# Performance work log

Hardware: AMD Instinct MI355X
Metric: run time of the kernel (lower is better)

The kernel has to match this reference:

```python
import jax, jax.numpy as jnp
import numpy as np
from jax import lax

K = 100
NUM_CLASSES = 80
MIN_X = 1; MIN_Y = 1; MAX_X = 4; MAX_Y = 4   # int(base_layer_range/16) for [16,64,16,64]
KEEP = 300
IOU_TH = 0.5
ROI_H = 2 * MAX_Y + 1  # 9
ROI_W = 2 * MAX_X + 1  # 9
MASK_OUT = 36          # 9 -> two stride-2 deconvs -> 36
SCALE = (36.0 - 1.0) / (9.0 - 1.0)
BN_INV = 1.0 / np.sqrt(1.0 + 1e-3)  # BN eval, running mean 0 / var 1, eps=1e-3
SIZES = [(64, 64), (32, 32), (16, 16)]


def bilinear(img, xx, yy):
    # img [..., H, W]; xx, yy same shape S; border-clamped bilinear sample -> [..., *S]
    H, W = img.shape[-2], img.shape[-1]
    xx = jnp.clip(xx, 0.0, W - 1.0)
    yy = jnp.clip(yy, 0.0, H - 1.0)
    x0f = jnp.floor(xx); y0f = jnp.floor(yy)
    wx = xx - x0f; wy = yy - y0f
    x0 = x0f.astype(jnp.int32); y0 = y0f.astype(jnp.int32)
    x1 = jnp.minimum(x0 + 1, W - 1); y1 = jnp.minimum(y0 + 1, H - 1)
    v00 = img[..., y0, x0]; v01 = img[..., y0, x1]
    v10 = img[..., y1, x0]; v11 = img[..., y1, x1]
    return (1 - wy) * ((1 - wx) * v00 + wx * v01) + wy * ((1 - wx) * v10 + wx * v11)


def roi_align(feat, boxes):
    # feat [C,H,W], boxes [N,4] in feat coords -> [N,C,ROI_H,ROI_W] (sampling_ratio=1)
    n = boxes.shape[0]
    x1, y1, x2, y2 = boxes[:, 0], boxes[:, 1], boxes[:, 2], boxes[:, 3]
    jx = (jnp.arange(ROI_W, dtype=jnp.float32) + 0.5) / ROI_W
    jy = (jnp.arange(ROI_H, dtype=jnp.float32) + 0.5) / ROI_H
    gx = x1[:, None] + (x2 - x1)[:, None] * jx  # [N,ROI_W]
    gy = y1[:, None] + (y2 - y1)[:, None] * jy  # [N,ROI_H]
    xx = jnp.broadcast_to(gx[:, None, :], (n, ROI_H, ROI_W))
    yy = jnp.broadcast_to(gy[:, :, None], (n, ROI_H, ROI_W))
    out = bilinear(feat, xx, yy)  # [C,N,ROI_H,ROI_W]
    return jnp.transpose(out, (1, 0, 2, 3))


def crop_resize(masks, boxes):
    # masks [N,h,w], boxes [N,4] -> [N,MASK_OUT,MASK_OUT]
    n = boxes.shape[0]
    t = jnp.arange(MASK_OUT, dtype=jnp.float32) / (MASK_OUT - 1.0)
    x1, y1, x2, y2 = boxes[:, 0], boxes[:, 1], boxes[:, 2], boxes[:, 3]
    gx = x1[:, None] + (x2 - x1)[:, None] * t
    gy = y1[:, None] + (y2 - y1)[:, None] * t
    xx = jnp.broadcast_to(gx[:, None, :], (n, MASK_OUT, MASK_OUT))
    yy = jnp.broadcast_to(gy[:, :, None], (n, MASK_OUT, MASK_OUT))
    return jax.vmap(bilinear)(masks, xx, yy)


def nms_keep(boxes, scores):
    # greedy NMS, faithful to torchvision semantics; returns bool keep flags [N]
    n = boxes.shape[0]
    x1, y1, x2, y2 = boxes[:, 0], boxes[:, 1], boxes[:, 2], boxes[:, 3]
    area = (x2 - x1) * (y2 - y1)
    ix1 = jnp.maximum(x1[:, None], x1[None, :]); iy1 = jnp.maximum(y1[:, None], y1[None, :])
    ix2 = jnp.minimum(x2[:, None], x2[None, :]); iy2 = jnp.minimum(y2[:, None], y2[None, :])
    inter = jnp.clip(ix2 - ix1, 0.0) * jnp.clip(iy2 - iy1, 0.0)
    iou = inter / (area[:, None] + area[None, :] - inter + 1e-9)
    order = jnp.argsort(-scores)  # stable
    def step(carry, idx):
        supp, keep = carry
        k = jnp.logical_not(supp[idx])
        keep = keep.at[idx].set(k)
        supp = jnp.logical_or(supp, jnp.logical_and(k, iou[idx] > IOU_TH))
        return (supp, keep), None
    init = (jnp.zeros((n,), bool), jnp.zeros((n,), bool))
    (_, keep), _ = lax.scan(step, init, order)
    return keep


def _conv(x, w, b, pad):
    y = lax.conv_general_dilated(x, w, (1, 1), [(pad, pad), (pad, pad)],
                                 dimension_numbers=('NCHW', 'OIHW', 'NCHW'))
    return y + b[None, :, None, None]


def _deconv(x, w, b):
    # ConvTranspose2d(k=2, s=2): fractionally-strided conv, doubles spatial size
    y = lax.conv_general_dilated(x, w, (1, 1), [(1, 1), (1, 1)], lhs_dilation=(2, 2),
                                 dimension_numbers=('NCHW', 'OIHW', 'NCHW'))
    return y + b[None, :, None, None]


def _bn(x, g, b):
    return x * (g * BN_INV)[None, :, None, None] + b[None, :, None, None]


def mask_head(x, c1_w, c1_b, mid_w, mid_b, bn_g, bn_b, d1_w, d1_b, d2_w, d2_b, c5_w, c5_b, c6_w, c6_b):
    r = jax.nn.relu
    h = r(_bn(_conv(x, c1_w, c1_b, 1), bn_g[0], bn_b[0]))
    for j in range(3):  # conv2..conv4
        h = r(_bn(_conv(h, mid_w[j], mid_b[j], 1), bn_g[1 + j], bn_b[1 + j]))
    h = r(_deconv(h, d1_w, d1_b))
    h = r(_bn(_conv(h, c5_w, c5_b, 1), bn_g[4], bn_b[4]))
    h = r(_deconv(h, d2_w, d2_b))
    return jax.nn.sigmoid(_conv(h, c6_w, c6_b, 0))


def _decode_layer(heat, tlr, brr, i, H0, W0):
    C, H, W = heat.shape
    hw = H * W
    scores, inds = lax.top_k(heat.reshape(-1), K)
    clses = (inds // hw).astype(jnp.float32)
    rem = inds % hw
    ys = (rem // W).astype(jnp.float32)
    xs = (rem % W).astype(jnp.float32)
    t = tlr.reshape(2, hw)[:, rem]  # [2,K]
    b = brr.reshape(2, hw)[:, rem]
    rx = float(MAX_X - MIN_X); ry = float(MAX_Y - MIN_Y)
    cx = (MAX_X + MIN_X) / 2.0;  cy = (MAX_Y + MIN_Y) / 2.0
    tlx = jnp.clip(xs - (rx * t[0] + cx), 0.0, float(W))
    tly = jnp.clip(ys - (ry * t[1] + cy), 0.0, float(H))
    brx = jnp.clip(xs + (rx * b[0] + cx), 0.0, float(W))
    bry = jnp.clip(ys + (ry * b[1] + cy), 0.0, float(H))
    boxes = jnp.stack([tlx, tly, brx, bry], 1)
    sc = jnp.where((brx < tlx) | (bry < tly), -1.0, scores)
    mb = jnp.stack([xs - MAX_X, ys - MAX_Y, xs + MAX_X, ys + MAX_Y,
                    jnp.full((K,), float(i))], 1)
    s2, order = lax.top_k(sc, K)  # num_dets(1000) >= K -> full sort by score
    boxes = boxes[order]; mb = mb[order]; cls = clses[order]
    lay = jnp.full((K,), float(i))
    cols = jnp.stack([s2, s2, lay, cls], 1)
    bws = jnp.concatenate([boxes, cols], 1)  # boxes_without_scaling [K,8]
    scale = jnp.array([W0 / W, H0 / H, W0 / W, H0 / H], jnp.float32)
    dets = jnp.concatenate([boxes * scale, cols], 1)
    return dets, bws, mb


def _decode_one(h0, h1, h2, t0, t1, t2, b0, b1, b2, f0, f1, f2,
                c1_w, c1_b, mid_w, mid_b, bn_g, bn_b, d1_w, d1_b, d2_w, d2_b,
                c5_w, c5_b, c6_w, c6_b):
    heats = (h0, h1, h2); tls = (t0, t1, t2); brs = (b0, b1, b2); feats = (f0, f1, f2)
    H0, W0 = heats[0].shape[1], heats[0].shape[2]
    dets_l, bws_l, mb_l = [], [], []
    for i in range(3):
        d, bw, mb = _decode_layer(heats[i], tls[i], brs[i], i, H0, W0)
        dets_l.append(d); bws_l.append(bw); mb_l.append(mb)
    dets = jnp.concatenate(dets_l, 0)   # [300,8]
    bws = jnp.concatenate(bws_l, 0)
    mb = jnp.concatenate(mb_l, 0)       # [300,5]
    # NMS faithful to source: boxes = detections[:,1:5], scores = detections[:,4]
    keep = nms_keep(dets[:, 1:5], dets[:, 4])
    sel = jnp.argsort(-jnp.where(keep, dets[:, 4], -1e9))[:KEEP]
    dets = dets[sel]; bws = bws[sel]; mb = mb[sel]
    # sort by mask layer index descending (features processed last->first)
    ord2 = jnp.argsort(-mb[:, 4])
    dets = dets[ord2]; bws = bws[ord2]; mb = mb[ord2]
    # ROI pool each box from its own layer's feature map
    pooled = jnp.stack([roi_align(feats[i], mb[:, :4]) for i in range(3)], 0)  # [3,N,C,9,9]
    lay = jnp.clip(mb[:, 4].astype(jnp.int32), 0, 2)
    rois = pooled[lay, jnp.arange(KEEP)]  # [N,256,9,9]
    masks_all = mask_head(rois, c1_w, c1_b, mid_w, mid_b, bn_g, bn_b,
                          d1_w, d1_b, d2_w, d2_b, c5_w, c5_b, c6_w, c6_b)  # [N,80,36,36]
    cls = jnp.clip(dets[:, 7].astype(jnp.int32), 0, NUM_CLASSES - 1)
    masks = masks_all[jnp.arange(KEEP), cls]  # [N,36,36] (one-hot scatter/select)
    bws4 = bws[:, :4] - jnp.tile(mb[:, :2], (1, 2))
    norm_boxes = SCALE * bws4
    masks = crop_resize(masks, norm_boxes)
    return dets, masks


def setup_inputs():
    key = jax.random.key(0)
    ks = jax.random.split(key, 32)
    B = 1
    inp = {}
    for i, (H, W) in enumerate(SIZES):
        inp['heat%d' % i] = jax.random.uniform(ks[i], (B, NUM_CLASSES, H, W), jnp.float32)
        inp['tl%d' % i] = 0.1 * jax.random.normal(ks[3 + i], (B, 2, H, W), jnp.float32)
        inp['br%d' % i] = 0.1 * jax.random.normal(ks[6 + i], (B, 2, H, W), jnp.float32)
        inp['feat%d' % i] = jax.random.normal(ks[9 + i], (B, 256, H, W), jnp.float32)
    inp['c1_w'] = 0.05 * jax.random.normal(ks[12], (256, 256, 3, 3), jnp.float32)
    inp['c1_b'] = jnp.zeros((256,), jnp.float32)
    inp['mid_w'] = 0.05 * jax.random.normal(ks[13], (3, 256, 256, 3, 3), jnp.float32)
    inp['mid_b'] = jnp.zeros((3, 256), jnp.float32)
    inp['bn_g'] = jnp.ones((5, 256), jnp.float32)
    inp['bn_b'] = jnp.zeros((5, 256), jnp.float32)
    inp['d1_w'] = 0.05 * jax.random.normal(ks[14], (256, 256, 2, 2), jnp.float32)
    inp['d1_b'] = jnp.zeros((256,), jnp.float32)
    inp['d2_w'] = 0.05 * jax.random.normal(ks[15], (256, 256, 2, 2), jnp.float32)
    inp['d2_b'] = jnp.zeros((256,), jnp.float32)
    inp['c5_w'] = 0.05 * jax.random.normal(ks[16], (256, 256, 3, 3), jnp.float32)
    inp['c5_b'] = jnp.zeros((256,), jnp.float32)
    inp['c6_w'] = 0.05 * jax.random.normal(ks[17], (NUM_CLASSES, 256, 1, 1), jnp.float32)
    inp['c6_b'] = jnp.zeros((NUM_CLASSES,), jnp.float32)
    return inp


def reference(heat0, heat1, heat2, tl0, tl1, tl2, br0, br1, br2, feat0, feat1, feat2,
              c1_w, c1_b, mid_w, mid_b, bn_g, bn_b, d1_w, d1_b, d2_w, d2_b,
              c5_w, c5_b, c6_w, c6_b):
    dets, masks = jax.vmap(_decode_one, in_axes=(0,) * 12 + (None,) * 14)(
        heat0, heat1, heat2, tl0, tl1, tl2, br0, br1, br2, feat0, feat1, feat2,
        c1_w, c1_b, mid_w, mid_b, bn_g, bn_b, d1_w, d1_b, d2_w, d2_b, c5_w, c5_b, c6_w, c6_b)
    return dets, masks  # [B,300,8], [B,300,36,36]
```

## Files before the change

### kernel.cpp

```cpp
#include <hip/hip_runtime.h>
#include <math.h>

typedef __attribute__((ext_vector_type(8))) short bf16x8;
typedef __attribute__((ext_vector_type(4))) float f32x4;

__device__ __forceinline__ unsigned fkey_u(float v){
  unsigned b = __float_as_uint(v);
  return (b & 0x80000000u) ? ~b : (b | 0x80000000u);
}
__device__ __forceinline__ float fkey_inv(unsigned m){
  unsigned b = (m & 0x80000000u) ? (m & 0x7fffffffu) : ~m;
  return __uint_as_float(b);
}
__device__ __forceinline__ unsigned short f2bf(float f){
  unsigned u = __float_as_uint(f);
  unsigned r = (u + 0x7fffu + ((u>>16)&1u)) >> 16;
  return (unsigned short)r;
}
__device__ __forceinline__ unsigned long long shfl_xor_u64(unsigned long long v, int mask){
  int lo = __shfl_xor((int)(unsigned)(v & 0xFFFFFFFFull), mask, 64);
  int hi = __shfl_xor((int)(unsigned)(v >> 32), mask, 64);
  return ((unsigned long long)(unsigned)hi << 32) | (unsigned long long)(unsigned)lo;
}
__device__ __forceinline__ unsigned long long bshfl_u64(unsigned long long v, int lane){
  int lo = __shfl((int)(unsigned)(v & 0xFFFFFFFFull), lane, 64);
  int hi = __shfl((int)(unsigned)(v >> 32), lane, 64);
  return ((unsigned long long)(unsigned)hi << 32) | (unsigned long long)(unsigned)lo;
}
#define BNI 0.9995003746877732f

template<int E, int J>
__device__ __forceinline__ void reg_step(unsigned long long* key, int t, int k2){
  #pragma unroll
  for (int r=0;r<E;r++){
    if ((r & J)==0){
      int e = t*E + r;
      bool desc = ((e & k2)==0);
      unsigned long long a=key[r], b=key[r^J];
      if (desc ? (a<b) : (a>b)){ key[r]=b; key[r^J]=a; }
    }
  }
}
template<int E>
__device__ __forceinline__ void reg_tail(unsigned long long* key, int t, int k2, int jstart){
  if constexpr (E>=8) { if (jstart>=4) reg_step<E,4>(key,t,k2); }
  if constexpr (E>=4) { if (jstart>=2) reg_step<E,2>(key,t,k2); }
  if (jstart>=1) reg_step<E,1>(key,t,k2);
}
template<int E>
__device__ void bitonic_desc(unsigned long long* key, unsigned long long* lds){
  const int t = threadIdx.x;
  const int N = E*256;
  for (int k2=2;k2<=N;k2<<=1){
    for (int j=k2>>1; j>=E; j>>=1){
      int w = j/E;
      bool lower = ((t & w)==0);
      bool desc  = (((t*E) & k2)==0);
      bool keep_max = (desc == lower);
      if (w < 64){
        #pragma unroll
        for (int r=0;r<E;r++){
          unsigned long long mine=key[r];
          unsigned long long o=shfl_xor_u64(mine, w);
          bool gt = mine > o;
          key[r] = keep_max ? (gt?mine:o) : (gt?o:mine);
        }
      } else {
        __syncthreads();
        #pragma unroll
        for (int r=0;r<E;r++) lds[t*E+r]=key[r];
        __syncthreads();
        #pragma unroll
        for (int r=0;r<E;r++){
          unsigned long long mine=key[r];
          unsigned long long o=lds[(t*E+r)^j];
          bool gt = mine > o;
          key[r] = keep_max ? (gt?mine:o) : (gt?o:mine);
        }
      }
    }
    int jstart = ((k2>>1) < (E>>1)) ? (k2>>1) : (E>>1);
    reg_tail<E>(key,t,k2,jstart);
  }
  __syncthreads();
  #pragma unroll
  for (int r=0;r<E;r++) lds[t*E+r]=key[r];
  __syncthreads();
}

__global__ __launch_bounds__(256) void k_sel1(
    const float* __restrict__ h0, const float* __restrict__ h1, const float* __restrict__ h2,
    unsigned long long* __restrict__ c1)
{
  int b = blockIdx.x;
  int layer, chunk;
  if (b < 320){ layer=0; chunk=b; }
  else if (b < 400){ layer=1; chunk=b-320; }
  else { layer=2; chunk=b-400; }
  const float* heat = (layer==0)?h0:((layer==1)?h1:h2);
  __shared__ unsigned long long lds[1024];
  unsigned long long key[4];
  int t = threadIdx.x;
  int base = chunk*1024 + t*4;
  float4 v = *(const float4*)(heat + base);
  key[0] = ((unsigned long long)fkey_u(v.x)<<32) | (unsigned long long)(0xFFFFFFFFu - (unsigned)(base+0));
  key[1] = ((unsigned long long)fkey_u(v.y)<<32) | (unsigned long long)(0xFFFFFFFFu - (unsigned)(base+1));
  key[2] = ((unsigned long long)fkey_u(v.z)<<32) | (unsigned long long)(0xFFFFFFFFu - (unsigned)(base+2));
  key[3] = ((unsigned long long)fkey_u(v.w)<<32) | (unsigned long long)(0xFFFFFFFFu - (unsigned)(base+3));
  bitonic_desc<4>(key, lds);
  if (t<100) c1[(size_t)b*100 + t] = lds[t];
}

__global__ __launch_bounds__(256) void k_sel2(
    const unsigned long long* __restrict__ c1, unsigned long long* __restrict__ c2)
{
  int b = blockIdx.x;
  __shared__ unsigned long long lds[2048];
  unsigned long long key[8];
  int t=threadIdx.x;
  const unsigned long long* src = c1 + (size_t)b*2000;
  #pragma unroll
  for (int r=0;r<8;r++){
    int i=t*8+r;
    key[r] = (i<2000)? src[i] : 0ull;
  }
  bitonic_desc<8>(key, lds);
  if (t<100) c2[(size_t)b*100+t]=lds[t];
}

__global__ __launch_bounds__(256) void k_sel3_decode(
    const unsigned long long* __restrict__ c2,
    const float* __restrict__ tl0,const float* __restrict__ tl1,const float* __restrict__ tl2,
    const float* __restrict__ br0,const float* __restrict__ br1,const float* __restrict__ br2,
    float* __restrict__ dets, float* __restrict__ bws, float* __restrict__ mbw)
{
  int layer = blockIdx.x;
  int hw = 4096 >> (layer*2);
  int W = 64>>layer;
  float Wf = (float)W;
  const float* tl = (layer==0)?tl0:((layer==1)?tl1:tl2);
  const float* br = (layer==0)?br0:((layer==1)?br1:br2);
  int base = (layer==0)?0:((layer==1)?1600:2000);
  int cnt  = (layer==0)?1600:((layer==1)?400:100);
  __shared__ unsigned long long lds[2048];
  __shared__ float scl[100];
  unsigned long long key[8];
  int t = threadIdx.x;
  #pragma unroll
  for (int r=0;r<8;r++){
    int i=t*8+r;
    key[r] = (i<cnt)? c2[base+i] : 0ull;
  }
  bitonic_desc<8>(key, lds);
  unsigned long long kwin=0;
  if (t<100) kwin = lds[t];
  float tlx=0,tly=0,brx=0,bry=0,xs=0,ys=0,clsfv=0,scv=0;
  if (t<100){
    unsigned m=(unsigned)(kwin>>32);
    unsigned gidx = 0xFFFFFFFFu - (unsigned)(kwin & 0xFFFFFFFFull);
    float val = fkey_inv(m);
    int cls = (int)(gidx / (unsigned)hw);
    int rem = (int)(gidx % (unsigned)hw);
    int iy = rem / W, ix = rem % W;
    xs = (float)ix; ys = (float)iy; clsfv = (float)cls;
    float t0=tl[rem], t1=tl[hw+rem], b0=br[rem], b1=br[hw+rem];
    tlx = fminf(fmaxf(xs - (3.0f*t0 + 2.5f), 0.0f), Wf);
    tly = fminf(fmaxf(ys - (3.0f*t1 + 2.5f), 0.0f), Wf);
    brx = fminf(fmaxf(xs + (3.0f*b0 + 2.5f), 0.0f), Wf);
    bry = fminf(fmaxf(ys + (3.0f*b1 + 2.5f), 0.0f), Wf);
    scv = ((brx<tlx)||(bry<tly)) ? -1.0f : val;
    scl[t]=scv;
  }
  __syncthreads();
  if (t<100){
    int rank=0;
    for (int i=0;i<100;i++){
      float si=scl[i];
      rank += ((si>scv)||(si==scv && i<t)) ? 1 : 0;
    }
    int row = layer*100 + rank;
    float sx = (float)(1<<layer);
    float* dr = dets + row*8;
    dr[0]=tlx*sx; dr[1]=tly*sx; dr[2]=brx*sx; dr[3]=bry*sx;
    dr[4]=scv; dr[5]=scv; dr[6]=(float)layer; dr[7]=clsfv;
    float* bwr = bws + row*8;
    bwr[0]=tlx;bwr[1]=tly;bwr[2]=brx;bwr[3]=bry;bwr[4]=scv;bwr[5]=scv;bwr[6]=(float)layer;bwr[7]=clsfv;
    float* mr = mbw + row*5;
    mr[0]=xs-4.0f; mr[1]=ys-4.0f; mr[2]=xs+4.0f; mr[3]=ys+4.0f; mr[4]=(float)layer;
  }
}

#define NMS_STEP(P, OC, M) { \
  int idx=__shfl((OC),(P),64); \
  unsigned long long supw=bshfl_u64(sup, idx>>6); \
  int kq=(int)((~(supw>>(idx&63)))&1ull); \
  if (t==0) keep_[idx]=kq; \
  unsigned long long v0=bshfl_u64(M[0],(P)); \
  unsigned long long v1=bshfl_u64(M[1],(P)); \
  unsigned long long v2=bshfl_u64(M[2],(P)); \
  unsigned long long v3=bshfl_u64(M[3],(P)); \
  unsigned long long v4=bshfl_u64(M[4],(P)); \
  unsigned long long mv=(t==0)?v0:((t==1)?v1:((t==2)?v2:((t==3)?v3:((t==4)?v4:0ull)))); \
  if (kq) sup|=mv; }

__global__ __launch_bounds__(320) void k_nms(
    const float* __restrict__ dets, const float* __restrict__ bws, const float* __restrict__ mbw,
    float* __restrict__ out_dets, float* __restrict__ mbf, int* __restrict__ clsf,
    int* __restrict__ layf, float* __restrict__ nbox)
{
  __shared__ __align__(16) float4 bq[300];
  __shared__ __align__(16) float sc[300];
  __shared__ __align__(16) float kk[300];
  __shared__ __align__(16) float lq[300];
  __shared__ float lyv[300];
  __shared__ unsigned long long sm_ord[300][5];
  __shared__ int order_[300], keep_[300], sel_[300], fperm[300];
  int t = threadIdx.x;
  float X1=0,Y1=0,X2=0,Y2=0,S=0,A=0;
  if (t<300){
    const float* r = dets + t*8;
    X1=r[1];Y1=r[2];X2=r[3];Y2=r[4];
    S=r[4];
    A=(X2-X1)*(Y2-Y1);
    bq[t]=make_float4(X1,Y1,X2,Y2);
    sc[t]=S;
    lyv[t]=mbw[t*5+4];
  }
  __syncthreads();
  if (t<300){
    int rank=0;
    for (int j4=0;j4<75;j4++){
      float4 s4=*(const float4*)&sc[j4*4];
      int j=j4*4;
      rank += ((s4.x>S)||(s4.x==S&&(j+0)<t)) ? 1:0;
      rank += ((s4.y>S)||(s4.y==S&&(j+1)<t)) ? 1:0;
      rank += ((s4.z>S)||(s4.z==S&&(j+2)<t)) ? 1:0;
      rank += ((s4.w>S)||(s4.w==S&&(j+3)<t)) ? 1:0;
    }
    unsigned long long wrow[5];
    #pragma unroll
    for (int jw=0;jw<5;jw++){
      unsigned long long bits=0;
      int lim=(jw==4)?44:64;
      for (int jj=0;jj<lim;jj++){
        int j=jw*64+jj;
        float4 q=bq[j];
        float aj=(q.z-q.x)*(q.w-q.y);
        float ix1=fmaxf(X1,q.x), iy1=fmaxf(Y1,q.y);
        float ix2=fminf(X2,q.z), iy2=fminf(Y2,q.w);
        float it=fmaxf(ix2-ix1,0.f)*fmaxf(iy2-iy1,0.f);
        float iou=it/(A+aj-it+1e-9f);
        bits |= ((unsigned long long)(iou>0.5f))<<jj;
      }
      wrow[jw]=bits;
    }
    order_[rank]=t;
    #pragma unroll
    for (int q=0;q<5;q++) sm_ord[rank][q]=wrow[q];
  }
  __syncthreads();
  if (t<64){
    int o0=order_[t], o1=order_[64+t], o2=order_[128+t], o3=order_[192+t];
    int o4=(t<44)? order_[256+t] : 0;
    unsigned long long m0[5],m1[5],m2[5],m3[5],m4[5];
    #pragma unroll
    for (int q=0;q<5;q++){
      m0[q]=sm_ord[t][q]; m1[q]=sm_ord[64+t][q];
      m2[q]=sm_ord[128+t][q]; m3[q]=sm_ord[192+t][q];
      m4[q]=(t<44)? sm_ord[256+t][q] : 0ull;
    }
    unsigned long long sup=0;
    for (int p=0;p<64;p++) NMS_STEP(p,o0,m0);
    for (int p=0;p<64;p++) NMS_STEP(p,o1,m1);
    for (int p=0;p<64;p++) NMS_STEP(p,o2,m2);
    for (int p=0;p<64;p++) NMS_STEP(p,o3,m3);
    for (int p=0;p<44;p++) NMS_STEP(p,o4,m4);
  }
  __syncthreads();
  if (t<300) kk[t] = keep_[t] ? sc[t] : -1000000000.0f;
  __syncthreads();
  float KV=0; int rank2=0;
  if (t<300){
    KV=kk[t];
    for (int j4=0;j4<75;j4++){
      float4 s4=*(const float4*)&kk[j4*4];
      int j=j4*4;
      rank2 += ((s4.x>KV)||(s4.x==KV&&(j+0)<t)) ? 1:0;
      rank2 += ((s4.y>KV)||(s4.y==KV&&(j+1)<t)) ? 1:0;
      rank2 += ((s4.z>KV)||(s4.z==KV&&(j+2)<t)) ? 1:0;
      rank2 += ((s4.w>KV)||(s4.w==KV&&(j+3)<t)) ? 1:0;
    }
    sel_[rank2]=t;
  }
  __syncthreads();
  if (t<300) lq[t]=lyv[sel_[t]];
  __syncthreads();
  if (t<300){
    float L=lq[t]; int rank3=0;
    for (int j4=0;j4<75;j4++){
      float4 s4=*(const float4*)&lq[j4*4];
      int j=j4*4;
      rank3 += ((s4.x>L)||(s4.x==L&&(j+0)<t)) ? 1:0;
      rank3 += ((s4.y>L)||(s4.y==L&&(j+1)<t)) ? 1:0;
      rank3 += ((s4.z>L)||(s4.z==L&&(j+2)<t)) ? 1:0;
      rank3 += ((s4.w>L)||(s4.w==L&&(j+3)<t)) ? 1:0;
    }
    fperm[rank3]=sel_[t];
  }
  __syncthreads();
  if (t<300){
    int src=fperm[t];
    const float* dr=dets+src*8;
    #pragma unroll
    for (int c=0;c<8;c++) out_dets[t*8+c]=dr[c];
    const float* mr=mbw+src*5;
    #pragma unroll
    for (int c=0;c<5;c++) mbf[t*5+c]=mr[c];
    int cc=(int)dr[7]; cc = cc<0?0:(cc>79?79:cc); clsf[t]=cc;
    int lv=(int)mr[4]; lv = lv<0?0:(lv>2?2:lv); layf[t]=lv;
    const float* bw=bws+src*8;
    nbox[t*4+0]=4.375f*(bw[0]-mr[0]);
    nbox[t*4+1]=4.375f*(bw[1]-mr[1]);
    nbox[t*4+2]=4.375f*(bw[2]-mr[0]);
    nbox[t*4+3]=4.375f*(bw[3]-mr[1]);
  }
}

__global__ __launch_bounds__(64) void k_wprep3(
    const float* __restrict__ c1w, const float* __restrict__ midw, const float* __restrict__ c5w,
    unsigned short* __restrict__ WB)
{
  int b = blockIdx.x, c = blockIdx.y, l = threadIdx.x;
  int t = b>>7;
  const float* src = (c==0)? c1w : (c<=3 ? midw + (size_t)(c-1)*589824 : c5w);
  unsigned short* dst = WB + (size_t)c*589824 + ((size_t)b<<9) + l*8;
  int co = (b&15)*16 + (l&15);
  int cib = ((b>>4)&7)*32 + ((l>>4)<<3);
  #pragma unroll
  for (int j=0;j<8;j++) dst[j] = f2bf(src[((size_t)co*256 + cib + j)*9 + t]);
}
__global__ __launch_bounds__(64) void k_wprep2(
    const float* __restrict__ d1w, const float* __restrict__ d2w,
    unsigned short* __restrict__ WD)
{
  int b = blockIdx.x, c = blockIdx.y, l = threadIdx.x;
  int t = b>>7;
  const float* src = (c==0)? d1w : d2w;
  unsigned short* dst = WD + (size_t)c*262144 + ((size_t)b<<9) + l*8;
  int co = (b&15)*16 + (l&15);
  int cib = ((b>>4)&7)*32 + ((l>>4)<<3);
  #pragma unroll
  for (int j=0;j<8;j++) dst[j] = f2bf(src[((size_t)co*256 + cib + j)*4 + t]);
}

__global__ __launch_bounds__(512,1) void k_mconv9x4(
    const float* __restrict__ f0,const float* __restrict__ f1,const float* __restrict__ f2,
    const float* __restrict__ mbf, const int* __restrict__ layf,
    const unsigned short* __restrict__ WB,
    const float* __restrict__ c1b, const float* __restrict__ midb,
    const float* __restrict__ bng, const float* __restrict__ bnb,
    unsigned short* __restrict__ B9, int r0)
{
  __shared__ __align__(16) unsigned short bufA[82*264];
  __shared__ __align__(16) unsigned short bufB[82*264];
  __shared__ int ix0[9], ix1[9], iy0[9], iy1[9];
  __shared__ float wxs[9], wys[9];
  int tid=threadIdx.x, l=tid&63, w=tid>>6;
  int g=r0+blockIdx.x;
  int lay=layf[g];
  int W=64>>lay;
  float Wf1=(float)(W-1);
  const float* feat=(lay==0)?f0:((lay==1)?f1:f2);
  if (tid<9){
    float x1=mbf[g*5+0], x2=mbf[g*5+2];
    float jx=((float)tid+0.5f)/9.0f;
    float gx=x1+(x2-x1)*jx;
    float xx=fminf(fmaxf(gx,0.0f),Wf1);
    float x0f=floorf(xx);
    wxs[tid]=xx-x0f;
    int x0=(int)x0f; ix0[tid]=x0; ix1[tid]=min(x0+1,W-1);
  } else if (tid>=16 && tid<25){
    int j=tid-16;
    float y1=mbf[g*5+1], y2=mbf[g*5+3];
    float jy=((float)j+0.5f)/9.0f;
    float gy=y1+(y2-y1)*jy;
    float yy=fminf(fmaxf(gy,0.0f),Wf1);
    float y0f=floorf(yy);
    wys[j]=yy-y0f;
    int y0=(int)y0f; iy0[j]=y0; iy1[j]=min(y0+1,W-1);
  }
  if (tid<264){ bufA[81*264+tid]=0; bufB[81*264+tid]=0; }
  __syncthreads();
  {
    int c=tid&255, h=tid>>8;
    const float* fp=feat+(size_t)c*W*W;
    int p0=h?41:0, p1=h?81:41;
    for (int p=p0;p<p1;p++){
      int py=p/9, px=p%9;
      float v00=fp[iy0[py]*W+ix0[px]];
      float v01=fp[iy0[py]*W+ix1[px]];
      float v10=fp[iy1[py]*W+ix0[px]];
      float v11=fp[iy1[py]*W+ix1[px]];
      float wxx=wxs[px], wyy=wys[py];
      float v=(1.0f-wyy)*((1.0f-wxx)*v00+wxx*v01)+wyy*((1.0f-wxx)*v10+wxx*v11);
      bufA[p*264+c]=f2bf(v);
    }
  }
  __syncthreads();
  int ym[6], xm[6];
  #pragma unroll
  for (int mt=0;mt<6;mt++){
    int m=mt*16+(l&15); if(m>80)m=80;
    ym[mt]=m/9; xm[mt]=m%9;
  }
  int kg=(l>>4)<<3;
  int rb=(l>>4)<<2;
  for (int L=0;L<4;L++){
    const unsigned short* inb=(L&1)?bufB:bufA;
    unsigned short* outb=(L&1)?bufA:bufB;
    const unsigned short* WL=WB+(size_t)L*589824+(size_t)l*8;
    const float* Bc=(L==0)?c1b:(midb+(size_t)(L-1)*256);
    const float* Gm=bng+(size_t)L*256;
    const float* Bn=bnb+(size_t)L*256;
    f32x4 acc[6][2] = {};
    for (int t9=0;t9<9;t9++){
      int dy=t9/3-1, dx=t9%3-1;
      int rowi[6];
      #pragma unroll
      for (int mt=0;mt<6;mt++){
        int y=ym[mt]+dy, x=xm[mt]+dx;
        rowi[mt]=((unsigned)y<9u&&(unsigned)x<9u)?(y*9+x):81;
      }
      for (int kc=0;kc<8;kc++){
        bf16x8 a[6],b[2];
        #pragma unroll
        for (int mt=0;mt<6;mt++) a[mt]=*(const bf16x8*)&inb[rowi[mt]*264+(kc<<5)+kg];
        #pragma unroll
        for (int nn=0;nn<2;nn++) b[nn]=*(const bf16x8*)(WL+((size_t)(((t9<<3)+kc)*16+(w<<1)+nn)<<9));
        #pragma unroll
        for (int mt=0;mt<6;mt++){
          #pragma unroll
          for (int nn=0;nn<2;nn++)
            acc[mt][nn]=__builtin_amdgcn_mfma_f32_16x16x32_bf16(a[mt],b[nn],acc[mt][nn],0,0,0);
        }
      }
    }
    #pragma unroll
    for (int nn=0;nn<2;nn++){
      int co=(w<<5)+(nn<<4)+(l&15);
      float bc=Bc[co], gm=Gm[co]*BNI, bb=Bn[co];
      #pragma unroll
      for (int mt=0;mt<6;mt++){
        #pragma unroll
        for (int r=0;r<4;r++){
          int m=mt*16+rb+r;
          if (m<81) outb[m*264+co]=f2bf(fmaxf((acc[mt][nn][r]+bc)*gm+bb,0.f));
        }
      }
    }
    __syncthreads();
  }
  unsigned short* Yr=B9+(size_t)blockIdx.x*81*256;
  for (int idx=tid; idx<81*32; idx+=512){
    int p=idx>>5, c8=(idx&31)<<3;
    *(uint4*)(Yr+p*256+c8)=*(const uint4*)&bufA[p*264+c8];
  }
}

__global__ __launch_bounds__(256,2) void k_mdeconv1(
    const unsigned short* __restrict__ Xg, unsigned short* __restrict__ Yg,
    const unsigned short* __restrict__ WD1, const float* __restrict__ Bd)
{
  __shared__ __align__(16) unsigned short Xp[81*264];
  int tid=threadIdx.x, l=tid&63, w=tid>>6;
  int tp=blockIdx.y;
  const unsigned short* Xr = Xg + (size_t)blockIdx.x*81*256;
  for (int idx=tid; idx<81*32; idx+=256){
    int pp=idx>>5, k8=idx&31;
    *(uint4*)&Xp[pp*264+(k8<<3)] = *(const uint4*)(Xr + (pp<<8)+(k8<<3));
  }
  __syncthreads();
  int pixb[6];
  #pragma unroll
  for (int mt=0;mt<6;mt++){ int m=mt*16+(l&15); pixb[mt]=(m>80)?80:m; }
  int kg=(l>>4)<<3;
  f32x4 acc[6][4] = {};
  const unsigned short* wbase = WD1 + (size_t)tp*65536 + (size_t)l*8;
  for (int kc=0;kc<8;kc++){
    bf16x8 a[6], b[4];
    #pragma unroll
    for (int mt=0;mt<6;mt++) a[mt] = *(const bf16x8*)&Xp[pixb[mt]*264 + (kc<<5) + kg];
    #pragma unroll
    for (int nn=0;nn<4;nn++) b[nn] = *(const bf16x8*)(wbase + ((size_t)(kc*16 + (w<<2)+nn)<<9));
    #pragma unroll
    for (int mt=0;mt<6;mt++){
      #pragma unroll
      for (int nn=0;nn<4;nn++)
        acc[mt][nn] = __builtin_amdgcn_mfma_f32_16x16x32_bf16(a[mt], b[nn], acc[mt][nn], 0,0,0);
    }
  }
  unsigned short* Yr = Yg + (size_t)blockIdx.x*324*256;
  int ky=tp>>1, kx=tp&1;
  int rb=(l>>4)<<2;
  #pragma unroll
  for (int nn=0;nn<4;nn++){
    int co=(w<<6)+(nn<<4)+(l&15);
    float bd=Bd[co];
    #pragma unroll
    for (int mt=0;mt<6;mt++){
      #pragma unroll
      for (int r=0;r<4;r++){
        int m=mt*16+rb+r;
        if (m<81){
          int iy=m/9, ix=m%9;
          int opx=(2*iy+1-ky)*18 + (2*ix+1-kx);
          Yr[opx*256+co]=f2bf(fmaxf(acc[mt][nn][r]+bd,0.f));
        }
      }
    }
  }
}

__global__ __launch_bounds__(256,2) void k_mconv18(
    const unsigned short* __restrict__ Xg, unsigned short* __restrict__ Yg,
    const unsigned short* __restrict__ WBc,
    const float* __restrict__ Bc, const float* __restrict__ Gg, const float* __restrict__ Bn)
{
  __shared__ __align__(16) unsigned short Xp[160*136];
  int tid=threadIdx.x, l=tid&63, w=tid>>6;
  int rg=blockIdx.y, ch=blockIdx.z;
  const unsigned short* Xr = Xg + (size_t)blockIdx.x*324*256;
  int pixb[7];
  #pragma unroll
  for (int mt=0;mt<7;mt++){ int m=mt*16+(l&15); if(m>107)m=107; pixb[mt]=(m/18)*20+(m%18); }
  int kg=(l>>4)<<3;
  f32x4 acc[7][2] = {};
  const unsigned short* wbase = WBc + (size_t)l*8;
  for (int h=0;h<2;h++){
    __syncthreads();
    for (int idx=tid; idx<160*16; idx+=256){
      int pp=idx>>4, k8=idx&15;
      int py=rg*6-1+pp/20, px=pp%20-1;
      uint4 v{0,0,0,0};
      if ((unsigned)py<18u && (unsigned)px<18u)
        v = *(const uint4*)(Xr + ((py*18+px)<<8) + (h<<7) + (k8<<3));
      *(uint4*)&Xp[pp*136 + (k8<<3)] = v;
    }
    __syncthreads();
    for (int t9=0;t9<9;t9++){
      int toff=(t9/3)*20 + (t9%3);
      for (int kc=0;kc<4;kc++){
        int kcg=(h<<2)+kc;
        bf16x8 a[7], b[2];
        #pragma unroll
        for (int mt=0;mt<7;mt++) a[mt] = *(const bf16x8*)&Xp[(pixb[mt]+toff)*136 + (kc<<5) + kg];
        #pragma unroll
        for (int nn=0;nn<2;nn++) b[nn] = *(const bf16x8*)(wbase + ((size_t)(((t9<<3)+kcg)*16 + (ch<<3)+(w<<1)+nn)<<9));
        #pragma unroll
        for (int mt=0;mt<7;mt++){
          #pragma unroll
          for (int nn=0;nn<2;nn++)
            acc[mt][nn] = __builtin_amdgcn_mfma_f32_16x16x32_bf16(a[mt], b[nn], acc[mt][nn], 0,0,0);
        }
      }
    }
  }
  unsigned short* Yr = Yg + (size_t)blockIdx.x*324*256;
  int rb=(l>>4)<<2;
  #pragma unroll
  for (int nn=0;nn<2;nn++){
    int co=(ch<<7)+(w<<5)+(nn<<4)+(l&15);
    float bc=Bc[co], gm=Gg[co]*BNI, bb=Bn[co];
    #pragma unroll
    for (int mt=0;mt<7;mt++){
      #pragma unroll
      for (int r=0;r<4;r++){
        int m=mt*16+rb+r;
        if (m<108){
          int opx=rg*108+m;
          Yr[opx*256+co]=f2bf(fmaxf((acc[mt][nn][r]+bc)*gm+bb, 0.f));
        }
      }
    }
  }
}

__global__ __launch_bounds__(256,2) void k_mdec2c6(
    const unsigned short* __restrict__ Xg,
    const unsigned short* __restrict__ WD2, const float* __restrict__ Bd,
    const float* __restrict__ W6, const float* __restrict__ B6,
    const int* __restrict__ clsf, float* __restrict__ mask36, int r0)
{
  __shared__ __align__(16) unsigned short Xp[108*264];
  __shared__ float part[4][112];
  int tid=threadIdx.x, l=tid&63, w=tid>>6;
  int tp=blockIdx.y, rg=blockIdx.z;
  int g=r0+blockIdx.x;
  const unsigned short* Xr = Xg + (size_t)blockIdx.x*324*256 + (size_t)rg*108*256;
  for (int idx=tid; idx<108*32; idx+=256){
    int pp=idx>>5, k8=idx&31;
    *(uint4*)&Xp[pp*264+(k8<<3)] = *(const uint4*)(Xr + (pp<<8)+(k8<<3));
  }
  __syncthreads();
  int pixb[7];
  #pragma unroll
  for (int mt=0;mt<7;mt++){ int m=mt*16+(l&15); pixb[mt]=(m>107)?107:m; }
  int kg=(l>>4)<<3;
  f32x4 acc[7][4] = {};
  const unsigned short* wbase = WD2 + (size_t)tp*65536 + (size_t)l*8;
  for (int kc=0;kc<8;kc++){
    bf16x8 a[7], b[4];
    #pragma unroll
    for (int mt=0;mt<7;mt++) a[mt] = *(const bf16x8*)&Xp[pixb[mt]*264 + (kc<<5) + kg];
    #pragma unroll
    for (int nn=0;nn<4;nn++) b[nn] = *(const bf16x8*)(wbase + ((size_t)(kc*16 + (w<<2)+nn)<<9));
    #pragma unroll
    for (int mt=0;mt<7;mt++){
      #pragma unroll
      for (int nn=0;nn<4;nn++)
        acc[mt][nn] = __builtin_amdgcn_mfma_f32_16x16x32_bf16(a[mt], b[nn], acc[mt][nn], 0,0,0);
    }
  }
  int cls=clsf[g];
  float w6v[4], bdv[4];
  #pragma unroll
  for (int nn=0;nn<4;nn++){
    int co=(w<<6)+(nn<<4)+(l&15);
    w6v[nn]=W6[(size_t)cls*256+co];
    bdv[nn]=Bd[co];
  }
  int rb=(l>>4)<<2;
  #pragma unroll
  for (int mt=0;mt<7;mt++){
    float s0=0.f,s1=0.f,s2=0.f,s3=0.f;
    #pragma unroll
    for (int nn=0;nn<4;nn++){
      s0 += fmaxf(acc[mt][nn][0]+bdv[nn],0.f)*w6v[nn];
      s1 += fmaxf(acc[mt][nn][1]+bdv[nn],0.f)*w6v[nn];
      s2 += fmaxf(acc[mt][nn][2]+bdv[nn],0.f)*w6v[nn];
      s3 += fmaxf(acc[mt][nn][3]+bdv[nn],0.f)*w6v[nn];
    }
    #pragma unroll
    for (int o=1;o<16;o<<=1){
      s0 += __shfl_xor(s0,o,64);
      s1 += __shfl_xor(s1,o,64);
      s2 += __shfl_xor(s2,o,64);
      s3 += __shfl_xor(s3,o,64);
    }
    if ((l&15)==0){
      int mb=mt*16+rb;
      part[w][mb+0]=s0; part[w][mb+1]=s1; part[w][mb+2]=s2; part[w][mb+3]=s3;
    }
  }
  __syncthreads();
  if (tid<108){
    float lg = part[0][tid]+part[1][tid]+part[2][tid]+part[3][tid] + B6[cls];
    int pg=rg*108+tid, iy=pg/18, ix=pg%18;
    int ky=tp>>1, kx=tp&1;
    mask36[(size_t)g*1296 + (2*iy+1-ky)*36 + (2*ix+1-kx)] = 1.0f/(1.0f+expf(-lg));
  }
}

__global__ __launch_bounds__(256) void k_crop(
    const float* __restrict__ mask36, const float* __restrict__ nbox,
    float* __restrict__ outm)
{
  int r=blockIdx.x;
  __shared__ float m[1296];
  int t=threadIdx.x;
  for (int i=t;i<1296;i+=256) m[i]=mask36[(size_t)r*1296+i];
  float x1=nbox[r*4+0], y1=nbox[r*4+1], x2=nbox[r*4+2], y2=nbox[r*4+3];
  __syncthreads();
  for (int p=t;p<1296;p+=256){
    int oy=p/36, ox=p%36;
    float tx=(float)ox/35.0f, ty=(float)oy/35.0f;
    float gx=x1+(x2-x1)*tx, gy=y1+(y2-y1)*ty;
    float xx=fminf(fmaxf(gx,0.f),35.0f), yy=fminf(fmaxf(gy,0.f),35.0f);
    float x0f=floorf(xx), y0f=floorf(yy);
    float wxv=xx-x0f, wyv=yy-y0f;
    int x0=(int)x0f, y0=(int)y0f;
    int x1i=min(x0+1,35), y1i=min(y0+1,35);
    float v00=m[y0*36+x0], v01=m[y0*36+x1i], v10=m[y1i*36+x0], v11=m[y1i*36+x1i];
    outm[(size_t)r*1296+p]=(1.f-wyv)*((1.f-wxv)*v00+wxv*v01)+wyv*((1.f-wxv)*v10+wxv*v11);
  }
}

extern "C" void kernel_launch(void* const* d_in, const int* in_sizes, int n_in,
                              void* d_out, int out_size, void* d_ws, size_t ws_size,
                              hipStream_t stream) {
  int iH[3], iT[3], iB[3], iF[3];
  if (n_in >= 12 && in_sizes[1] == 2*64*64) {
    for (int l=0;l<3;l++){ iH[l]=l*4+0; iT[l]=l*4+1; iB[l]=l*4+2; iF[l]=l*4+3; }
  } else {
    for (int l=0;l<3;l++){ iH[l]=l; iT[l]=3+l; iB[l]=6+l; iF[l]=9+l; }
  }
  const float* heat0=(const float*)d_in[iH[0]];
  const float* heat1=(const float*)d_in[iH[1]];
  const float* heat2=(const float*)d_in[iH[2]];
  const float* tl0=(const float*)d_in[iT[0]];
  const float* tl1=(const float*)d_in[iT[1]];
  const float* tl2=(const float*)d_in[iT[2]];
  const float* br0=(const float*)d_in[iB[0]];
  const float* br1=(const float*)d_in[iB[1]];
  const float* br2=(const float*)d_in[iB[2]];
  const float* feat0=(const float*)d_in[iF[0]];
  const float* feat1=(const float*)d_in[iF[1]];
  const float* feat2=(const float*)d_in[iF[2]];
  const float* c1w=(const float*)d_in[12];
  const float* c1b=(const float*)d_in[13];
  const float* midw=(const float*)d_in[14];
  const float* midb=(const float*)d_in[15];
  const float* bng=(const float*)d_in[16];
  const float* bnb=(const float*)d_in[17];
  const float* d1w=(const float*)d_in[18];
  const float* d1b=(const float*)d_in[19];
  const float* d2w=(const float*)d_in[20];
  const float* d2b=(const float*)d_in[21];
  const float* c5w=(const float*)d_in[22];
  const float* c5b=(const float*)d_in[23];
  const float* c6w=(const float*)d_in[24];
  const float* c6b=(const float*)d_in[25];
  float* out=(float*)d_out;

  char* ws=(char*)d_ws;
  size_t cur=0;
  auto alloc=[&](size_t bytes)->char*{
    char* p=ws+cur;
    cur=(cur+bytes+255)&~(size_t)255;
    return p;
  };
  unsigned short* WB=(unsigned short*)alloc(5ull*589824*2);
  unsigned short* WD=(unsigned short*)alloc(2ull*262144*2);
  unsigned long long* c1s=(unsigned long long*)alloc(420ull*100*8);
  unsigned long long* c2s=(unsigned long long*)alloc(21ull*100*8);
  float* detsw=(float*)alloc(300*8*4);
  float* bwsw=(float*)alloc(300*8*4);
  float* mbw=(float*)alloc(300*5*4);
  float* mbf=(float*)alloc(300*5*4);
  int* clsf=(int*)alloc(300*4);
  int* layf=(int*)alloc(300*4);
  float* nbox=(float*)alloc(300*4*4);
  float* mask36=(float*)alloc(300ull*1296*4);
  size_t fixed=cur;
  size_t perroi = (size_t)(81 + 2*324)*256*2;
  size_t avail = (ws_size>fixed+4096)? (ws_size-fixed-4096):0;
  int NRC = (int)(avail/perroi);
  if (NRC>300) NRC=300;
  if (NRC<1) NRC=1;
  unsigned short* B9 =(unsigned short*)alloc((size_t)NRC*81*256*2);
  unsigned short* C18=(unsigned short*)alloc((size_t)NRC*324*256*2);
  unsigned short* D18=(unsigned short*)alloc((size_t)NRC*324*256*2);

  k_wprep3<<<dim3(1152,5),dim3(64),0,stream>>>(c1w,midw,c5w,WB);
  k_wprep2<<<dim3(512,2),dim3(64),0,stream>>>(d1w,d2w,WD);

  k_sel1<<<dim3(420),dim3(256),0,stream>>>(heat0,heat1,heat2,c1s);
  k_sel2<<<dim3(21),dim3(256),0,stream>>>(c1s,c2s);
  k_sel3_decode<<<dim3(3),dim3(256),0,stream>>>(c2s,tl0,tl1,tl2,br0,br1,br2,detsw,bwsw,mbw);
  k_nms<<<dim3(1),dim3(320),0,stream>>>(detsw,bwsw,mbw,out,mbf,clsf,layf,nbox);

  for (int r0=0;r0<300;r0+=NRC){
    int nr = (300-r0 < NRC)? (300-r0) : NRC;
    k_mconv9x4<<<dim3(nr),dim3(512),0,stream>>>(feat0,feat1,feat2,mbf,layf,WB,c1b,midb,bng,bnb,B9,r0);
    k_mdeconv1<<<dim3(nr,4),dim3(256),0,stream>>>(B9,C18,WD,d1b);
    k_mconv18<<<dim3(nr,3,2),dim3(256),0,stream>>>(C18,D18,WB+4ull*589824, c5b, bng+1024, bnb+1024);
    k_mdec2c6<<<dim3(nr,4,3),dim3(256),0,stream>>>(D18,WD+262144,d2b,c6w,c6b,clsf,mask36,r0);
  }
  k_crop<<<dim3(300),dim3(256),0,stream>>>(mask36,nbox,out+2400);
}
```

Before: 769.6 us.

## Split fused 4-layer 9x9 conv into ROI kernel plus per-layer half-tile convs

```diff
diff --git a/kernel.cpp b/kernel.cpp
--- a/kernel.cpp
+++ b/kernel.cpp
@@ -326,6 +326,53 @@
   }
 }
 
+__global__ __launch_bounds__(256) void k_roi(
+    const float* __restrict__ f0,const float* __restrict__ f1,const float* __restrict__ f2,
+    const float* __restrict__ mbf, const int* __restrict__ layf,
+    unsigned short* __restrict__ rois, int r0)
+{
+  int nl = blockIdx.x; int g = r0 + nl;
+  __shared__ int ix0[9], ix1[9], iy0[9], iy1[9];
+  __shared__ float wx[9], wy[9];
+  int lay = layf[g];
+  int W = 64>>lay;
+  float Wf1 = (float)(W-1);
+  const float* feat = (lay==0)?f0:((lay==1)?f1:f2);
+  int t=threadIdx.x;
+  if (t<9){
+    float x1=mbf[g*5+0], x2=mbf[g*5+2];
+    float jx = ((float)t + 0.5f)/9.0f;
+    float gx = x1 + (x2-x1)*jx;
+    float xx = fminf(fmaxf(gx,0.0f), Wf1);
+    float x0f = floorf(xx);
+    wx[t]=xx-x0f;
+    int x0=(int)x0f; ix0[t]=x0; ix1[t]=min(x0+1,W-1);
+  } else if (t>=16 && t<25){
+    int j=t-16;
+    float y1=mbf[g*5+1], y2=mbf[g*5+3];
+    float jy=((float)j+0.5f)/9.0f;
+    float gy=y1+(y2-y1)*jy;
+    float yy=fminf(fmaxf(gy,0.0f),Wf1);
+    float y0f=floorf(yy);
+    wy[j]=yy-y0f;
+    int y0=(int)y0f; iy0[j]=y0; iy1[j]=min(y0+1,W-1);
+  }
+  __syncthreads();
+  int c=t;
+  const float* fp = feat + (size_t)c*W*W;
+  unsigned short* op = rois + (size_t)nl*81*256;
+  for (int p=0;p<81;p++){
+    int py=p/9, px=p%9;
+    float v00=fp[iy0[py]*W+ix0[px]];
+    float v01=fp[iy0[py]*W+ix1[px]];
+    float v10=fp[iy1[py]*W+ix0[px]];
+    float v11=fp[iy1[py]*W+ix1[px]];
+    float wxx=wx[px], wyy=wy[py];
+    float v = (1.0f-wyy)*((1.0f-wxx)*v00 + wxx*v01) + wyy*((1.0f-wxx)*v10 + wxx*v11);
+    op[(size_t)p*256 + c] = f2bf(v);
+  }
+}
+
 __global__ __launch_bounds__(64) void k_wprep3(
     const float* __restrict__ c1w, const float* __restrict__ midw, const float* __restrict__ c5w,
     unsigned short* __restrict__ WB)
@@ -353,117 +400,69 @@
   for (int j=0;j<8;j++) dst[j] = f2bf(src[((size_t)co*256 + cib + j)*4 + t]);
 }
 
-__global__ __launch_bounds__(512,1) void k_mconv9x4(
-    const float* __restrict__ f0,const float* __restrict__ f1,const float* __restrict__ f2,
-    const float* __restrict__ mbf, const int* __restrict__ layf,
-    const unsigned short* __restrict__ WB,
-    const float* __restrict__ c1b, const float* __restrict__ midb,
-    const float* __restrict__ bng, const float* __restrict__ bnb,
-    unsigned short* __restrict__ B9, int r0)
-{
-  __shared__ __align__(16) unsigned short bufA[82*264];
-  __shared__ __align__(16) unsigned short bufB[82*264];
-  __shared__ int ix0[9], ix1[9], iy0[9], iy1[9];
-  __shared__ float wxs[9], wys[9];
+__global__ __launch_bounds__(256,3) void k_mconv9h(
+    const unsigned short* __restrict__ Xg, unsigned short* __restrict__ Yg,
+    const unsigned short* __restrict__ WBc,
+    const float* __restrict__ Bc, const float* __restrict__ Gg, const float* __restrict__ Bn)
+{
+  __shared__ __align__(16) unsigned short Xp[88*264];
   int tid=threadIdx.x, l=tid&63, w=tid>>6;
-  int g=r0+blockIdx.x;
-  int lay=layf[g];
-  int W=64>>lay;
-  float Wf1=(float)(W-1);
-  const float* feat=(lay==0)?f0:((lay==1)?f1:f2);
-  if (tid<9){
-    float x1=mbf[g*5+0], x2=mbf[g*5+2];
-    float jx=((float)tid+0.5f)/9.0f;
-    float gx=x1+(x2-x1)*jx;
-    float xx=fminf(fmaxf(gx,0.0f),Wf1);
-    float x0f=floorf(xx);
-    wxs[tid]=xx-x0f;
-    int x0=(int)x0f; ix0[tid]=x0; ix1[tid]=min(x0+1,W-1);
-  } else if (tid>=16 && tid<25){
-    int j=tid-16;
-    float y1=mbf[g*5+1], y2=mbf[g*5+3];
-    float jy=((float)j+0.5f)/9.0f;
-    float gy=y1+(y2-y1)*jy;
-    float yy=fminf(fmaxf(gy,0.0f),Wf1);
-    float y0f=floorf(yy);
-    wys[j]=yy-y0f;
-    int y0=(int)y0f; iy0[j]=y0; iy1[j]=min(y0+1,W-1);
-  }
-  if (tid<264){ bufA[81*264+tid]=0; bufB[81*264+tid]=0; }
-  __syncthreads();
-  {
-    int c=tid&255, h=tid>>8;
-    const float* fp=feat+(size_t)c*W*W;
-    int p0=h?41:0, p1=h?81:41;
-    for (int p=p0;p<p1;p++){
-      int py=p/9, px=p%9;
-      float v00=fp[iy0[py]*W+ix0[px]];
-      float v01=fp[iy0[py]*W+ix1[px]];
-      float v10=fp[iy1[py]*W+ix0[px]];
-      float v11=fp[iy1[py]*W+ix1[px]];
-      float wxx=wxs[px], wyy=wys[py];
-      float v=(1.0f-wyy)*((1.0f-wxx)*v00+wxx*v01)+wyy*((1.0f-wxx)*v10+wxx*v11);
-      bufA[p*264+c]=f2bf(v);
-    }
-  }
-  __syncthreads();
-  int ym[6], xm[6];
-  #pragma unroll
-  for (int mt=0;mt<6;mt++){
-    int m=mt*16+(l&15); if(m>80)m=80;
-    ym[mt]=m/9; xm[mt]=m%9;
+  int h=blockIdx.y;
+  int rlo = h ? 4 : -1;
+  const unsigned short* Xr = Xg + (size_t)blockIdx.x*81*256;
+  for (int idx=tid; idx<88*32; idx+=256){
+    int pp=idx>>5, k8=idx&31;
+    int y=pp/11 + rlo, x=pp%11 - 1;
+    uint4 v{0,0,0,0};
+    if ((unsigned)y<9u && (unsigned)x<9u) v = *(const uint4*)(Xr + ((y*9+x)<<8) + (k8<<3));
+    *(uint4*)&Xp[pp*264 + (k8<<3)] = v;
+  }
+  __syncthreads();
+  int mbase = h*48;
+  int pixb[3];
+  #pragma unroll
+  for (int mt=0;mt<3;mt++){
+    int m=mbase+mt*16+(l&15); if(m>80)m=80;
+    pixb[mt]=(m/9 - rlo)*11 + (m%9) + 1;
   }
   int kg=(l>>4)<<3;
+  f32x4 acc[3][4] = {};
+  const unsigned short* wbase = WBc + (size_t)l*8;
+  for (int t9=0;t9<9;t9++){
+    int toff=(t9/3-1)*11 + (t9%3-1);
+    for (int kc=0;kc<8;kc++){
+      bf16x8 a[3], b[4];
+      #pragma unroll
+      for (int mt=0;mt<3;mt++) a[mt] = *(const bf16x8*)&Xp[(pixb[mt]+toff)*264 + (kc<<5) + kg];
+      #pragma unroll
+      for (int nn=0;nn<4;nn++) b[nn] = *(const bf16x8*)(wbase + ((size_t)(((t9<<3)+kc)*16 + (w<<2)+nn)<<9));
+      #pragma unroll
+      for (int mt=0;mt<3;mt++){
+        #pragma unroll
+        for (int nn=0;nn<4;nn++)
+          acc[mt][nn] = __builtin_amdgcn_mfma_f32_16x16x32_bf16(a[mt], b[nn], acc[mt][nn], 0,0,0);
+      }
+    }
+  }
+  unsigned short* Yr = Yg + (size_t)blockIdx.x*81*256;
   int rb=(l>>4)<<2;
-  for (int L=0;L<4;L++){
-    const unsigned short* inb=(L&1)?bufB:bufA;
-    unsigned short* outb=(L&1)?bufA:bufB;
-    const unsigned short* WL=WB+(size_t)L*589824+(size_t)l*8;
-    const float* Bc=(L==0)?c1b:(midb+(size_t)(L-1)*256);
-    const float* Gm=bng+(size_t)L*256;
-    const float* Bn=bnb+(size_t)L*256;
-    f32x4 acc[6][2] = {};
-    for (int t9=0;t9<9;t9++){
-      int dy=t9/3-1, dx=t9%3-1;
-      int rowi[6];
+  #pragma unroll
+  for (int nn=0;nn<4;nn++){
+    int co=(w<<6)+(nn<<4)+(l&15);
+    float bc=Bc[co], gm=Gg[co]*BNI, bb=Bn[co];
+    #pragma unroll
+    for (int mt=0;mt<3;mt++){
       #pragma unroll
-      for (int mt=0;mt<6;mt++){
-        int y=ym[mt]+dy, x=xm[mt]+dx;
-        rowi[mt]=((unsigned)y<9u&&(unsigned)x<9u)?(y*9+x):81;
-      }
-      for (int kc=0;kc<8;kc++){
-        bf16x8 a[6],b[2];
-        #pragma unroll
-        for (int mt=0;mt<6;mt++) a[mt]=*(const bf16x8*)&inb[rowi[mt]*264+(kc<<5)+kg];
-        #pragma unroll
-        for (int nn=0;nn<2;nn++) b[nn]=*(const bf16x8*)(WL+((size_t)(((t9<<3)+kc)*16+(w<<1)+nn)<<9));
-        #pragma unroll
-        for (int mt=0;mt<6;mt++){
-          #pragma unroll
-          for (int nn=0;nn<2;nn++)
-            acc[mt][nn]=__builtin_amdgcn_mfma_f32_16x16x32_bf16(a[mt],b[nn],acc[mt][nn],0,0,0);
+      for (int r=0;r<4;r++){
+        int m=mbase+mt*16+rb+r;
+        if (m<81 || h==0){
+          if (m<81){
+            float v=fmaxf((acc[mt][nn][r]+bc)*gm+bb, 0.f);
+            Yr[m*256+co]=f2bf(v);
+          }
         }
       }
     }
-    #pragma unroll
-    for (int nn=0;nn<2;nn++){
-      int co=(w<<5)+(nn<<4)+(l&15);
-      float bc=Bc[co], gm=Gm[co]*BNI, bb=Bn[co];
-      #pragma unroll
-      for (int mt=0;mt<6;mt++){
-        #pragma unroll
-        for (int r=0;r<4;r++){
-          int m=mt*16+rb+r;
-          if (m<81) outb[m*264+co]=f2bf(fmaxf((acc[mt][nn][r]+bc)*gm+bb,0.f));
-        }
-      }
-    }
-    __syncthreads();
-  }
-  unsigned short* Yr=B9+(size_t)blockIdx.x*81*256;
-  for (int idx=tid; idx<81*32; idx+=512){
-    int p=idx>>5, c8=(idx&31)<<3;
-    *(uint4*)(Yr+p*256+c8)=*(const uint4*)&bufA[p*264+c8];
   }
 }
 
@@ -742,11 +741,12 @@
   float* nbox=(float*)alloc(300*4*4);
   float* mask36=(float*)alloc(300ull*1296*4);
   size_t fixed=cur;
-  size_t perroi = (size_t)(81 + 2*324)*256*2;
+  size_t perroi = (size_t)(2*81 + 2*324)*256*2;
   size_t avail = (ws_size>fixed+4096)? (ws_size-fixed-4096):0;
   int NRC = (int)(avail/perroi);
   if (NRC>300) NRC=300;
   if (NRC<1) NRC=1;
+  unsigned short* X0 =(unsigned short*)alloc((size_t)NRC*81*256*2);
   unsigned short* B9 =(unsigned short*)alloc((size_t)NRC*81*256*2);
   unsigned short* C18=(unsigned short*)alloc((size_t)NRC*324*256*2);
   unsigned short* D18=(unsigned short*)alloc((size_t)NRC*324*256*2);
@@ -761,8 +761,12 @@
 
   for (int r0=0;r0<300;r0+=NRC){
     int nr = (300-r0 < NRC)? (300-r0) : NRC;
-    k_mconv9x4<<<dim3(nr),dim3(512),0,stream>>>(feat0,feat1,feat2,mbf,layf,WB,c1b,midb,bng,bnb,B9,r0);
-    k_mdeconv1<<<dim3(nr,4),dim3(256),0,stream>>>(B9,C18,WD,d1b);
+    k_roi<<<dim3(nr),dim3(256),0,stream>>>(feat0,feat1,feat2,mbf,layf,X0,r0);
+    k_mconv9h<<<dim3(nr,2),dim3(256),0,stream>>>(X0,B9,WB,               c1b,       bng,      bnb);
+    k_mconv9h<<<dim3(nr,2),dim3(256),0,stream>>>(B9,X0,WB+1ull*589824,   midb,      bng+256,  bnb+256);
+    k_mconv9h<<<dim3(nr,2),dim3(256),0,stream>>>(X0,B9,WB+2ull*589824,   midb+256,  bng+512,  bnb+512);
+    k_mconv9h<<<dim3(nr,2),dim3(256),0,stream>>>(B9,X0,WB+3ull*589824,   midb+512,  bng+768,  bnb+768);
+    k_mdeconv1<<<dim3(nr,4),dim3(256),0,stream>>>(X0,C18,WD,d1b);
     k_mconv18<<<dim3(nr,3,2),dim3(256),0,stream>>>(C18,D18,WB+4ull*589824, c5b, bng+1024, bnb+1024);
     k_mdec2c6<<<dim3(nr,4,3),dim3(256),0,stream>>>(D18,WD+262144,d2b,c6w,c6b,clsf,mask36,r0);
   }
```

Result: faster. 696.2 us (-9.5%).
